# Performance work log

Hardware: AMD Instinct MI355X
Metric: run time of the kernel (lower is better)

Reference implementation:

```python
import jax, jax.numpy as jnp
import numpy as np


def _pos_enc(seq_len, d_model, dtype):
    # PositionalEncoding2D buffer: interleaved sin/cos, standard transformer PE
    pos = jnp.arange(seq_len, dtype=dtype)[:, None]                      # [S,1]
    div = jnp.exp(jnp.arange(0, d_model, 2, dtype=dtype) * (-(np.log(10000.0) / d_model)))  # [d/2]
    pe = jnp.zeros((seq_len, d_model), dtype=dtype)
    pe = pe.at[:, 0::2].set(jnp.sin(pos * div))
    pe = pe.at[:, 1::2].set(jnp.cos(pos * div))
    return pe


def setup_inputs() -> dict:
    key = jax.random.key(0)
    k1, k2 = jax.random.split(key)
    B, C, H, W = 32, 384, 32, 32
    d = C
    x = jax.random.normal(k1, (B, C, H, W), dtype=jnp.float32)
    # fused QKV projection weight (stored as [d, 3d] so y = x @ W + b)
    Wqkv = jax.random.normal(k2, (d, 3 * d), dtype=jnp.float32) * (1.0 / np.sqrt(d))
    b = jnp.zeros((3 * d,), dtype=jnp.float32)
    return {"x": x, "W": Wqkv, "b": b}


def reference(x, W, b):
    B, C, H, Wd = x.shape
    d = C
    S = H * Wd
    xs = x.reshape(B, C, S).transpose(0, 2, 1)          # [B,S,d]
    xs = xs + _pos_enc(S, d, xs.dtype)                  # add positional encoding
    qkv = xs @ W + b                                    # [B,S,3d]
    q, k, v = jnp.split(qkv, 3, axis=-1)                # each [B,S,d]
    scores = jnp.einsum('bqd,bkd->bqk', q, k) / (d ** 0.5)  # [B,S,S]
    attn = jax.nn.softmax(scores, axis=-1)
    weighted = jnp.einsum('bqk,bkd->bqd', attn, v)      # [B,S,d]
    return weighted.transpose(0, 2, 1).reshape(B, C, H, Wd)
```

## Files before the change

### kernel.cpp

```cpp
#include <hip/hip_runtime.h>
#include <hip/hip_bf16.h>
#include <math.h>

typedef __attribute__((ext_vector_type(8))) __bf16 bf16x8;
typedef __attribute__((ext_vector_type(4))) float f32x4;

#define S_LEN 1024
#define D_MODEL 384
#define BATCH 32
#define N3 1152
#define KVB 32
#define NT (S_LEN / KVB)

#define MFMA16(a, b, c) __builtin_amdgcn_mfma_f32_16x16x32_bf16((a), (b), (c), 0, 0, 0)

static __device__ __forceinline__ ushort f2bf(float f) {
    __bf16 h = (__bf16)f;
    return __builtin_bit_cast(ushort, h);
}
static __device__ __forceinline__ float exp2a(float x) {
    float r; asm("v_exp_f32 %0, %1" : "=v"(r) : "v"(x)); return r;
}
static __device__ __forceinline__ uint cvtpk(float a, float b) {
    uint r; asm("v_cvt_pk_bf16_f32 %0, %1, %2" : "=v"(r) : "v"(a), "v"(b)); return r;
}

__global__ void pe_kernel(float* peT) {
    int idx = blockIdx.x * 256 + threadIdx.x;
    int k = idx >> 10, s = idx & 1023;
    float e = -(float)((k >> 1) * 2) * (logf(10000.0f) / (float)D_MODEL);
    float div = expf(e);
    float a = (float)s * div;
    peT[idx] = (k & 1) ? cosf(a) : sinf(a);
}

__global__ void wt_kernel(const float* __restrict__ W, ushort* __restrict__ Wt) {
    __shared__ float tile[32][33];
    int n0 = blockIdx.x * 32, k0 = blockIdx.y * 32;
    int tx = threadIdx.x, ty = threadIdx.y;
#pragma unroll
    for (int r = 0; r < 4; ++r) {
        int kl = ty * 4 + r;
        tile[kl][tx] = W[(size_t)(k0 + kl) * N3 + n0 + tx];
    }
    __syncthreads();
#pragma unroll
    for (int r = 0; r < 4; ++r) {
        int nl = ty * 4 + r;
        Wt[(size_t)(n0 + nl) * D_MODEL + k0 + tx] = f2bf(tile[tx][nl]);
    }
}

__global__ __launch_bounds__(256) void astage_kernel(const float* __restrict__ x,
                                                     const float* __restrict__ peT,
                                                     ushort* __restrict__ A) {
    __shared__ ushort Ld[64 * 68];
    int sb = blockIdx.x, kb = blockIdx.y, b = blockIdx.z;
    int s0 = sb * 64, k0 = kb * 64;
    int t = threadIdx.x, l = t & 63, w = t >> 6;
    int sg = l & 15;
    const float4* x4 = (const float4*)x;
    const float4* p4 = (const float4*)peT;
#pragma unroll
    for (int r = 0; r < 4; ++r) {
        int kl = w * 4 + (l >> 4) + r * 16;
        int kg = k0 + kl;
        float4 v = x4[((size_t)(b * D_MODEL + kg) << 8) + sb * 16 + sg];
        float4 p = p4[((size_t)kg << 8) + sb * 16 + sg];
        ushort4 o;
        o.x = f2bf(v.x + p.x); o.y = f2bf(v.y + p.y);
        o.z = f2bf(v.z + p.z); o.w = f2bf(v.w + p.w);
        *reinterpret_cast<ushort4*>(&Ld[kl * 68 + sg * 4]) = o;
    }
    __syncthreads();
#pragma unroll
    for (int p = 0; p < 2; ++p) {
        int s_loc = (t >> 3) + p * 32;
        int kg = t & 7;
        ushort4 o0, o1;
        o0.x = Ld[(kg * 8 + 0) * 68 + s_loc]; o0.y = Ld[(kg * 8 + 1) * 68 + s_loc];
        o0.z = Ld[(kg * 8 + 2) * 68 + s_loc]; o0.w = Ld[(kg * 8 + 3) * 68 + s_loc];
        o1.x = Ld[(kg * 8 + 4) * 68 + s_loc]; o1.y = Ld[(kg * 8 + 5) * 68 + s_loc];
        o1.z = Ld[(kg * 8 + 6) * 68 + s_loc]; o1.w = Ld[(kg * 8 + 7) * 68 + s_loc];
        ushort* dst = A + (size_t)(b * S_LEN + s0 + s_loc) * D_MODEL + k0 + kg * 8;
        *reinterpret_cast<ushort4*>(dst) = o0;
        *reinterpret_cast<ushort4*>(dst + 4) = o1;
    }
}

__global__ __launch_bounds__(256) void qkv_gemm(const ushort* __restrict__ A,
                                                const ushort* __restrict__ Wt,
                                                const float* __restrict__ bias,
                                                ushort* __restrict__ Qb,
                                                ushort* __restrict__ Ktl,
                                                ushort* __restrict__ Vtl) {
    __shared__ __align__(16) ushort As[2][128 * 32];
    __shared__ __align__(16) ushort Bs[2][128 * 32];
    int id = blockIdx.x;
    int g = id / 288, loc = id % 288;
    int nt_ = loc / 32, mt_ = g * 32 + (loc % 32);
    int m0 = mt_ * 128, n0 = nt_ * 128;
    int tid = threadIdx.x;
    int wave = tid >> 6, lane = tid & 63;
    int i16 = lane & 15, gq = lane >> 4;
    int wr = wave >> 1, wc = wave & 1;

    auto stage = [&](int ks, int bi) {
        int k0 = ks * 32;
#pragma unroll
        for (int i = 0; i < 2; ++i) {
            int off = (wave * 2 + i) * 1024;
            int row = (off >> 6) + (lane >> 2);
            int kc = lane & 3;
            const ushort* ga = A + (size_t)(m0 + row) * D_MODEL + k0 + kc * 8;
            __builtin_amdgcn_global_load_lds(
                (const __attribute__((address_space(1))) uint32_t*)ga,
                (__attribute__((address_space(3))) uint32_t*)((char*)&As[bi][0] + off), 16, 0, 0);
            const ushort* gb = Wt + (size_t)(n0 + row) * D_MODEL + k0 + kc * 8;
            __builtin_amdgcn_global_load_lds(
                (const __attribute__((address_space(1))) uint32_t*)gb,
                (__attribute__((address_space(3))) uint32_t*)((char*)&Bs[bi][0] + off), 16, 0, 0);
        }
    };

    stage(0, 0);
    f32x4 acc[4][4] = {};
    for (int ks = 0; ks < 12; ++ks) {
        int bi = ks & 1;
        asm volatile("s_waitcnt vmcnt(0) lgkmcnt(0)" ::: "memory");
        __builtin_amdgcn_s_barrier();
        __builtin_amdgcn_sched_barrier(0);
        if (ks + 1 < 12) stage(ks + 1, bi ^ 1);
        bf16x8 af[4], bfr[4];
#pragma unroll
        for (int mt = 0; mt < 4; ++mt) {
            int row = wr * 64 + mt * 16 + i16;
            af[mt] = *reinterpret_cast<const bf16x8*>(&As[bi][row * 32 + gq * 8]);
        }
#pragma unroll
        for (int nt = 0; nt < 4; ++nt) {
            int row = wc * 64 + nt * 16 + i16;
            bfr[nt] = *reinterpret_cast<const bf16x8*>(&Bs[bi][row * 32 + gq * 8]);
        }
        __builtin_amdgcn_s_setprio(1);
#pragma unroll
        for (int mt = 0; mt < 4; ++mt)
#pragma unroll
            for (int nt = 0; nt < 4; ++nt)
                acc[mt][nt] = MFMA16(af[mt], bfr[nt], acc[mt][nt]);
        __builtin_amdgcn_s_setprio(0);
    }
    if (n0 < D_MODEL) {
#pragma unroll
        for (int nt = 0; nt < 4; ++nt) {
            int n = n0 + wc * 64 + nt * 16 + i16;
            float bv = bias[n];
#pragma unroll
            for (int mt = 0; mt < 4; ++mt)
#pragma unroll
                for (int r = 0; r < 4; ++r) {
                    int m = m0 + wr * 64 + mt * 16 + gq * 4 + r;
                    Qb[(size_t)m * D_MODEL + n] = f2bf(acc[mt][nt][r] + bv);
                }
        }
    } else if (n0 < 2 * D_MODEL) {
        int b = m0 >> 10;
#pragma unroll
        for (int nt = 0; nt < 4; ++nt) {
            int n = n0 + wc * 64 + nt * 16 + i16;
            float bv = bias[n];
            int k2 = n - D_MODEL;
            int slotk = k2 >> 3, within = k2 & 7;
#pragma unroll
            for (int mt = 0; mt < 4; ++mt)
#pragma unroll
                for (int r = 0; r < 4; ++r) {
                    int m = m0 + wr * 64 + mt * 16 + gq * 4 + r;
                    int s = m & 1023;
                    int t = s >> 5, j = s & 31;
                    size_t idx = (size_t)(b * 32 + t) * 12288 + j * 384
                               + (((slotk ^ (j & 7)) << 3) + within);
                    Ktl[idx] = f2bf(acc[mt][nt][r] + bv);
                }
        }
    } else {
        int b = m0 >> 10;
#pragma unroll
        for (int nt = 0; nt < 4; ++nt) {
            int n = n0 + wc * 64 + nt * 16 + i16;
            float bv = bias[n];
            int c = n - 2 * D_MODEL;
            int cx = (c >> 1) & 3;
#pragma unroll
            for (int mt = 0; mt < 4; ++mt) {
                int m = m0 + wr * 64 + mt * 16 + gq * 4;
                int s = m & 1023;
                int t = s >> 5, j = s & 31;
                size_t idx = (size_t)(b * 32 + t) * 12288 + c * 32
                           + ((((j >> 3) ^ cx) << 3) + (j & 7));
                ushort4 p4;
                p4.x = f2bf(acc[mt][nt][0] + bv);
                p4.y = f2bf(acc[mt][nt][1] + bv);
                p4.z = f2bf(acc[mt][nt][2] + bv);
                p4.w = f2bf(acc[mt][nt][3] + bv);
                *reinterpret_cast<ushort4*>(&Vtl[idx]) = p4;
            }
        }
    }
}

__global__ __launch_bounds__(768, 1) void attn_kernel(const ushort* __restrict__ Qb,
                                                      const ushort* __restrict__ Ktl,
                                                      const ushort* __restrict__ Vtl,
                                                      float* __restrict__ out) {
    __shared__ __align__(16) char smem[114688];
    int id = blockIdx.x;
    int xcd = id & 7, slot = (id >> 3) & 3, qt = id >> 5;
    int b = slot * 8 + xcd;
    int q0blk = qt * 128;
    int tid = threadIdx.x;
    int wave = tid >> 6, lane = tid & 63;
    int i16 = lane & 15, gq = lane >> 4;
    const float sl2e = 0.05103103630798287f * 1.4426950408889634f;

    auto stage_K = [&](int tt, int bi) {
        const ushort* pan = Ktl + (size_t)(b * 32 + tt) * 12288;
        char* dst = smem + bi * 24576;
#pragma unroll
        for (int r = 0; r < 2; ++r) {
            int ii = wave * 2 + r;
            const ushort* ga = pan + ii * 512 + lane * 8;
            __builtin_amdgcn_global_load_lds(
                (const __attribute__((address_space(1))) uint32_t*)ga,
                (__attribute__((address_space(3))) uint32_t*)(dst + ii * 1024), 16, 0, 0);
        }
    };
    auto stage_V = [&](int tt, int bi) {
        const ushort* pan = Vtl + (size_t)(b * 32 + tt) * 12288;
        char* dst = smem + 49152 + bi * 24576;
#pragma unroll
        for (int r = 0; r < 2; ++r) {
            int ii = wave * 2 + r;
            const ushort* ga = pan + ii * 512 + lane * 8;
            __builtin_amdgcn_global_load_lds(
                (const __attribute__((address_space(1))) uint32_t*)ga,
                (__attribute__((address_space(3))) uint32_t*)(dst + ii * 1024), 16, 0, 0);
        }
    };

    stage_K(0, 0);
    asm volatile("s_waitcnt vmcnt(0)" ::: "memory");
    __syncthreads();

    if (wave < 4) {
        int qg = wave;
        bf16x8 qf[12][2];
        const ushort* Q0 = Qb + (size_t)(b * S_LEN + q0blk + qg * 32 + i16) * D_MODEL;
        const ushort* Q1 = Q0 + (size_t)16 * D_MODEL;
#pragma unroll
        for (int kt = 0; kt < 12; ++kt) {
            qf[kt][0] = *reinterpret_cast<const bf16x8*>(Q0 + kt * 32 + gq * 8);
            qf[kt][1] = *reinterpret_cast<const bf16x8*>(Q1 + kt * 32 + gq * 8);
        }
        float lsum0 = 0.f, lsum1 = 0.f;
        int jc0 = gq >> 1, jc1 = 2 + (gq >> 1);
        int q0 = qg * 32 + i16, q1 = qg * 32 + 16 + i16;

        auto qk_step = [&](int tt) {
            const char* Kb = smem + (tt & 1) * 24576;
            char* Pw = smem + 98304 + (tt & 1) * 8192;
            f32x4 s00 = {}, s01 = {}, s10 = {}, s11 = {};
            __builtin_amdgcn_s_setprio(1);
#pragma unroll
            for (int kt = 0; kt < 12; ++kt) {
                int kc = (kt * 64 + gq * 16) ^ ((i16 & 7) << 4);
                bf16x8 kf0 = *reinterpret_cast<const bf16x8*>(Kb + i16 * 768 + kc);
                bf16x8 kf1 = *reinterpret_cast<const bf16x8*>(Kb + (16 + i16) * 768 + kc);
                s00 = MFMA16(kf0, qf[kt][0], s00);
                s01 = MFMA16(kf0, qf[kt][1], s01);
                s10 = MFMA16(kf1, qf[kt][0], s10);
                s11 = MFMA16(kf1, qf[kt][1], s11);
            }
            __builtin_amdgcn_s_setprio(0);
            {
                float p0 = exp2a(s00[0] * sl2e), p1 = exp2a(s00[1] * sl2e);
                float p2 = exp2a(s00[2] * sl2e), p3 = exp2a(s00[3] * sl2e);
                lsum0 += (p0 + p1) + (p2 + p3);
                uint2 w; w.x = cvtpk(p0, p1); w.y = cvtpk(p2, p3);
                *reinterpret_cast<uint2*>(Pw + jc0 * 2048 + ((q0 * 16) ^ ((jc0 & 3) << 4)) + (gq & 1) * 8) = w;
            }
            {
                float p0 = exp2a(s01[0] * sl2e), p1 = exp2a(s01[1] * sl2e);
                float p2 = exp2a(s01[2] * sl2e), p3 = exp2a(s01[3] * sl2e);
                lsum1 += (p0 + p1) + (p2 + p3);
                uint2 w; w.x = cvtpk(p0, p1); w.y = cvtpk(p2, p3);
                *reinterpret_cast<uint2*>(Pw + jc0 * 2048 + ((q1 * 16) ^ ((jc0 & 3) << 4)) + (gq & 1) * 8) = w;
            }
            {
                float p0 = exp2a(s10[0] * sl2e), p1 = exp2a(s10[1] * sl2e);
                float p2 = exp2a(s10[2] * sl2e), p3 = exp2a(s10[3] * sl2e);
                lsum0 += (p0 + p1) + (p2 + p3);
                uint2 w; w.x = cvtpk(p0, p1); w.y = cvtpk(p2, p3);
                *reinterpret_cast<uint2*>(Pw + jc1 * 2048 + ((q0 * 16) ^ ((jc1 & 3) << 4)) + (gq & 1) * 8) = w;
            }
            {
                float p0 = exp2a(s11[0] * sl2e), p1 = exp2a(s11[1] * sl2e);
                float p2 = exp2a(s11[2] * sl2e), p3 = exp2a(s11[3] * sl2e);
                lsum1 += (p0 + p1) + (p2 + p3);
                uint2 w; w.x = cvtpk(p0, p1); w.y = cvtpk(p2, p3);
                *reinterpret_cast<uint2*>(Pw + jc1 * 2048 + ((q1 * 16) ^ ((jc1 & 3) << 4)) + (gq & 1) * 8) = w;
            }
        };

        qk_step(0);
        stage_K(1, 1);
        stage_V(0, 0);
        asm volatile("s_waitcnt lgkmcnt(0)" ::: "memory");
        __builtin_amdgcn_s_barrier();
        for (int t = 0; t < NT; ++t) {
            asm volatile("s_waitcnt vmcnt(0) lgkmcnt(0)" ::: "memory");
            __builtin_amdgcn_s_barrier();
            __builtin_amdgcn_sched_barrier(0);
            if (t + 2 < NT) stage_K(t + 2, t & 1);
            if (t + 1 < NT) stage_V(t + 1, (t + 1) & 1);
            if (t + 1 < NT) qk_step(t + 1);
        }
        __syncthreads();
        lsum0 += __shfl_xor(lsum0, 16); lsum0 += __shfl_xor(lsum0, 32);
        lsum1 += __shfl_xor(lsum1, 16); lsum1 += __shfl_xor(lsum1, 32);
        float* Lt = reinterpret_cast<float*>(smem + 98304);
        if (gq == 0) {
            Lt[qg * 32 + i16] = lsum0;
            Lt[qg * 32 + 16 + i16] = lsum1;
        }
        __syncthreads();
    } else {
        int cs = wave - 4;
        f32x4 oc[3][8] = {};
        stage_K(1, 1);
        stage_V(0, 0);
        asm volatile("s_waitcnt lgkmcnt(0)" ::: "memory");
        __builtin_amdgcn_s_barrier();
        for (int t = 0; t < NT; ++t) {
            asm volatile("s_waitcnt vmcnt(0) lgkmcnt(0)" ::: "memory");
            __builtin_amdgcn_s_barrier();
            __builtin_amdgcn_sched_barrier(0);
            if (t + 2 < NT) stage_K(t + 2, t & 1);
            if (t + 1 < NT) stage_V(t + 1, (t + 1) & 1);
            const char* Vb = smem + 49152 + (t & 1) * 24576;
            const char* Pb = smem + 98304 + (t & 1) * 8192;
            bf16x8 pf[8];
#pragma unroll
            for (int qs = 0; qs < 8; ++qs) {
                int q = qs * 16 + i16;
                pf[qs] = *reinterpret_cast<const bf16x8*>(
                    Pb + gq * 2048 + ((q * 16) ^ ((gq & 3) << 4)));
            }
            __builtin_amdgcn_s_setprio(1);
#pragma unroll
            for (int ct = 0; ct < 3; ++ct) {
                int c = cs * 48 + ct * 16 + i16;
                bf16x8 vf = *reinterpret_cast<const bf16x8*>(
                    Vb + c * 64 + ((gq * 16) ^ (((i16 >> 1) & 3) << 4)));
                oc[ct][0] = MFMA16(vf, pf[0], oc[ct][0]);
                oc[ct][1] = MFMA16(vf, pf[1], oc[ct][1]);
                oc[ct][2] = MFMA16(vf, pf[2], oc[ct][2]);
                oc[ct][3] = MFMA16(vf, pf[3], oc[ct][3]);
                oc[ct][4] = MFMA16(vf, pf[4], oc[ct][4]);
                oc[ct][5] = MFMA16(vf, pf[5], oc[ct][5]);
                oc[ct][6] = MFMA16(vf, pf[6], oc[ct][6]);
                oc[ct][7] = MFMA16(vf, pf[7], oc[ct][7]);
            }
            __builtin_amdgcn_s_setprio(0);
        }
        __syncthreads();
        __syncthreads();
        const float* Lt = reinterpret_cast<const float*>(smem + 98304);
        float* ob = out + (size_t)b * D_MODEL * S_LEN + q0blk;
#pragma unroll
        for (int qs = 0; qs < 8; ++qs) {
            float inv = 1.0f / Lt[qs * 16 + i16];
#pragma unroll
            for (int ct = 0; ct < 3; ++ct)
#pragma unroll
                for (int r = 0; r < 4; ++r) {
                    int c = cs * 48 + ct * 16 + gq * 4 + r;
                    ob[(size_t)c * S_LEN + qs * 16 + i16] = oc[ct][qs][r] * inv;
                }
        }
    }
}

extern "C" void kernel_launch(void* const* d_in, const int* in_sizes, int n_in,
                              void* d_out, int out_size, void* d_ws, size_t ws_size,
                              hipStream_t stream) {
    const float* x    = (const float*)d_in[0];
    const float* W    = (const float*)d_in[1];
    const float* bias = (const float*)d_in[2];
    float* out = (float*)d_out;

    char* ws = (char*)d_ws;
    ushort* A_bf = (ushort*)(ws);
    ushort* Wt   = (ushort*)(ws + 25165824);
    float*  peT  = (float*)(ws + 26050560);
    ushort* Qb   = (ushort*)(ws + 27623424);
    ushort* Ktl  = (ushort*)(ws + 52789248);
    ushort* Vtl  = (ushort*)(ws + 77955072);

    pe_kernel<<<1536, 256, 0, stream>>>(peT);
    wt_kernel<<<dim3(36, 12), dim3(32, 8), 0, stream>>>(W, Wt);
    astage_kernel<<<dim3(16, 6, 32), 256, 0, stream>>>(x, peT, A_bf);
    qkv_gemm<<<2304, 256, 0, stream>>>(A_bf, Wt, bias, Qb, Ktl, Vtl);
    attn_kernel<<<256, 768, 0, stream>>>(Qb, Ktl, Vtl, out);
}
```

Measured before the change: 131.8 us.

## Widen QKV GEMM tile to 128x384 with 8 waves per block

The QKV projection GEMM now uses 128x384 output tiles computed by 512-thread blocks (8 waves, each 64x96), with 768 blocks in place of 2304 blocks of 128x128. Each A tile loaded into LDS is reused across three times as many output columns, cutting global/L2 traffic for the activation matrix. The block rasterisation now groups blocks by 4096-row chunks, and each block handles exactly one of Q, K or V. In exchange, shared memory grows to 64 KB per block and each wave holds 24 accumulators, which may reduce occupancy and leave fewer blocks to balance across CUs.

```diff
diff --git a/kernel.cpp b/kernel.cpp
--- a/kernel.cpp
+++ b/kernel.cpp
@@ -88,72 +88,76 @@
     }
 }
 
-__global__ __launch_bounds__(256) void qkv_gemm(const ushort* __restrict__ A,
-                                                const ushort* __restrict__ Wt,
-                                                const float* __restrict__ bias,
-                                                ushort* __restrict__ Qb,
-                                                ushort* __restrict__ Ktl,
-                                                ushort* __restrict__ Vtl) {
+__global__ __launch_bounds__(512, 2) void qkv_gemm(const ushort* __restrict__ A,
+                                                   const ushort* __restrict__ Wt,
+                                                   const float* __restrict__ bias,
+                                                   ushort* __restrict__ Qb,
+                                                   ushort* __restrict__ Ktl,
+                                                   ushort* __restrict__ Vtl) {
     __shared__ __align__(16) ushort As[2][128 * 32];
-    __shared__ __align__(16) ushort Bs[2][128 * 32];
+    __shared__ __align__(16) ushort Bs[2][384 * 32];
     int id = blockIdx.x;
-    int g = id / 288, loc = id % 288;
-    int nt_ = loc / 32, mt_ = g * 32 + (loc % 32);
-    int m0 = mt_ * 128, n0 = nt_ * 128;
+    int g = id / 96, loc = id % 96;
+    int nt_ = loc / 32, mt_ = loc % 32;
+    int m0 = g * 4096 + mt_ * 128, n0 = nt_ * 384;
     int tid = threadIdx.x;
     int wave = tid >> 6, lane = tid & 63;
     int i16 = lane & 15, gq = lane >> 4;
-    int wr = wave >> 1, wc = wave & 1;
+    int wr = wave >> 2, wc = wave & 3;
 
     auto stage = [&](int ks, int bi) {
         int k0 = ks * 32;
 #pragma unroll
-        for (int i = 0; i < 2; ++i) {
-            int off = (wave * 2 + i) * 1024;
-            int row = (off >> 6) + (lane >> 2);
-            int kc = lane & 3;
-            const ushort* ga = A + (size_t)(m0 + row) * D_MODEL + k0 + kc * 8;
-            __builtin_amdgcn_global_load_lds(
-                (const __attribute__((address_space(1))) uint32_t*)ga,
-                (__attribute__((address_space(3))) uint32_t*)((char*)&As[bi][0] + off), 16, 0, 0);
-            const ushort* gb = Wt + (size_t)(n0 + row) * D_MODEL + k0 + kc * 8;
-            __builtin_amdgcn_global_load_lds(
-                (const __attribute__((address_space(1))) uint32_t*)gb,
-                (__attribute__((address_space(3))) uint32_t*)((char*)&Bs[bi][0] + off), 16, 0, 0);
+        for (int j = 0; j < 4; ++j) {
+            int c = wave * 4 + j;
+            if (c < 8) {
+                int row = c * 16 + (lane >> 2);
+                const ushort* ga = A + (size_t)(m0 + row) * D_MODEL + k0 + (lane & 3) * 8;
+                __builtin_amdgcn_global_load_lds(
+                    (const __attribute__((address_space(1))) uint32_t*)ga,
+                    (__attribute__((address_space(3))) uint32_t*)((char*)&As[bi][0] + c * 1024), 16, 0, 0);
+            } else {
+                int row = (c - 8) * 16 + (lane >> 2);
+                const ushort* gb = Wt + (size_t)(n0 + row) * D_MODEL + k0 + (lane & 3) * 8;
+                __builtin_amdgcn_global_load_lds(
+                    (const __attribute__((address_space(1))) uint32_t*)gb,
+                    (__attribute__((address_space(3))) uint32_t*)((char*)&Bs[bi][0] + (c - 8) * 1024), 16, 0, 0);
+            }
         }
     };
 
     stage(0, 0);
-    f32x4 acc[4][4] = {};
+    f32x4 acc[4][6] = {};
     for (int ks = 0; ks < 12; ++ks) {
         int bi = ks & 1;
         asm volatile("s_waitcnt vmcnt(0) lgkmcnt(0)" ::: "memory");
         __builtin_amdgcn_s_barrier();
         __builtin_amdgcn_sched_barrier(0);
         if (ks + 1 < 12) stage(ks + 1, bi ^ 1);
-        bf16x8 af[4], bfr[4];
+        bf16x8 af[4], bfr[6];
 #pragma unroll
         for (int mt = 0; mt < 4; ++mt) {
             int row = wr * 64 + mt * 16 + i16;
             af[mt] = *reinterpret_cast<const bf16x8*>(&As[bi][row * 32 + gq * 8]);
         }
 #pragma unroll
-        for (int nt = 0; nt < 4; ++nt) {
-            int row = wc * 64 + nt * 16 + i16;
+        for (int nt = 0; nt < 6; ++nt) {
+            int row = wc * 96 + nt * 16 + i16;
             bfr[nt] = *reinterpret_cast<const bf16x8*>(&Bs[bi][row * 32 + gq * 8]);
         }
         __builtin_amdgcn_s_setprio(1);
 #pragma unroll
         for (int mt = 0; mt < 4; ++mt)
 #pragma unroll
-            for (int nt = 0; nt < 4; ++nt)
+            for (int nt = 0; nt < 6; ++nt)
                 acc[mt][nt] = MFMA16(af[mt], bfr[nt], acc[mt][nt]);
         __builtin_amdgcn_s_setprio(0);
     }
-    if (n0 < D_MODEL) {
-#pragma unroll
-        for (int nt = 0; nt < 4; ++nt) {
-            int n = n0 + wc * 64 + nt * 16 + i16;
+    int b = m0 >> 10;
+    if (n0 == 0) {
+#pragma unroll
+        for (int nt = 0; nt < 6; ++nt) {
+            int n = wc * 96 + nt * 16 + i16;
             float bv = bias[n];
 #pragma unroll
             for (int mt = 0; mt < 4; ++mt)
@@ -163,13 +167,11 @@
                     Qb[(size_t)m * D_MODEL + n] = f2bf(acc[mt][nt][r] + bv);
                 }
         }
-    } else if (n0 < 2 * D_MODEL) {
-        int b = m0 >> 10;
-#pragma unroll
-        for (int nt = 0; nt < 4; ++nt) {
-            int n = n0 + wc * 64 + nt * 16 + i16;
-            float bv = bias[n];
-            int k2 = n - D_MODEL;
+    } else if (n0 == D_MODEL) {
+#pragma unroll
+        for (int nt = 0; nt < 6; ++nt) {
+            int k2 = wc * 96 + nt * 16 + i16;
+            float bv = bias[D_MODEL + k2];
             int slotk = k2 >> 3, within = k2 & 7;
 #pragma unroll
             for (int mt = 0; mt < 4; ++mt)
@@ -184,12 +186,10 @@
                 }
         }
     } else {
-        int b = m0 >> 10;
-#pragma unroll
-        for (int nt = 0; nt < 4; ++nt) {
-            int n = n0 + wc * 64 + nt * 16 + i16;
-            float bv = bias[n];
-            int c = n - 2 * D_MODEL;
+#pragma unroll
+        for (int nt = 0; nt < 6; ++nt) {
+            int c = wc * 96 + nt * 16 + i16;
+            float bv = bias[2 * D_MODEL + c];
             int cx = (c >> 1) & 3;
 #pragma unroll
             for (int mt = 0; mt < 4; ++mt) {
@@ -410,6 +410,6 @@
     pe_kernel<<<1536, 256, 0, stream>>>(peT);
     wt_kernel<<<dim3(36, 12), dim3(32, 8), 0, stream>>>(W, Wt);
     astage_kernel<<<dim3(16, 6, 32), 256, 0, stream>>>(x, peT, A_bf);
-    qkv_gemm<<<2304, 256, 0, stream>>>(A_bf, Wt, bias, Qb, Ktl, Vtl);
+    qkv_gemm<<<768, 512, 0, stream>>>(A_bf, Wt, bias, Qb, Ktl, Vtl);
     attn_kernel<<<256, 768, 0, stream>>>(Qb, Ktl, Vtl, out);
 }
```

After: 128.6 us. 2.4% less time.
